# Performance work log

Hardware: AMD Instinct MI355X
Metric: run time of the kernel (lower is better)

Reference implementation:

```python
import jax, jax.numpy as jnp
import numpy as np

N = 50000      # nodes
E2 = 400000    # undirected edges
E = 2 * E2     # directed edges (each undirected edge in both directions)
DIN = 512      # input feature dim
DH = 128       # MLP hidden
C = 8          # num classes / BP channels


def setup_inputs() -> dict:
    key = jax.random.key(0)
    ks = jax.random.split(key, 9)
    x = jax.random.normal(ks[0], (N, DIN), jnp.float32)
    src0 = jax.random.randint(ks[1], (E2,), 0, N)
    dst0 = jax.random.randint(ks[2], (E2,), 0, N)
    # symmetric directed edge list: row 0 = source j, row 1 = target i
    edge_index = jnp.stack([jnp.concatenate([src0, dst0]),
                            jnp.concatenate([dst0, src0])])
    w0 = jax.random.uniform(ks[3], (E2,), jnp.float32, 0.5, 1.5)
    edge_weight = jnp.concatenate([w0, w0])  # reverse edge shares weight
    # edge_rv[e] = index of the reverse of edge e
    edge_rv = jnp.concatenate([jnp.arange(E2) + E2, jnp.arange(E2)])
    W1 = jax.random.normal(ks[4], (DIN, DH), jnp.float32) * 0.05
    b1 = jnp.zeros((DH,), jnp.float32)
    W2 = jax.random.normal(ks[5], (DH, C), jnp.float32) * 0.05
    b2 = jnp.zeros((C,), jnp.float32)
    param = jax.random.normal(ks[6], (C, C), jnp.float32) * 0.1
    return {"x": x, "edge_index": edge_index, "edge_weight": edge_weight,
            "edge_rv": edge_rv, "W1": W1, "b1": b1, "W2": W2, "b2": b2,
            "param": param, "K": 5}


def log_normalize(log_x):
    return log_x - jax.nn.logsumexp(log_x, axis=-1, keepdims=True)


def reference(x, edge_index, edge_weight, edge_rv, W1, b1, W2, b2, param, K):
    # MLP transform + LogSoftmax -> initial log-beliefs [N, C]
    h = jax.nn.relu(x @ W1 + b1)
    log_b0 = jax.nn.log_softmax(h @ W2 + b2, axis=-1)

    # learn_H=True: logH = logsigmoid(param + param^T), [C, C]
    logH = jax.nn.log_sigmoid(param + param.T)
    src, dst = edge_index[0], edge_index[1]
    # per-edge coupling matrix [E, C, C]
    logC = edge_weight[:, None, None] * logH[None, :, :]

    log_b = log_b0
    log_msg = None
    for _ in range(K):
        x_j = log_b[src]                       # gather source beliefs [E, C]
        if log_msg is not None:
            x_j = x_j - log_msg[edge_rv]       # remove reverse message
        # tropical-semiring matvec in log domain: logsumexp over source channel
        log_msg = log_normalize(jax.nn.logsumexp(x_j[:, :, None] + logC, axis=1))
        agg = jax.ops.segment_sum(log_msg, dst, num_segments=N)  # scatter-add
        log_b = log_normalize(log_b0 + agg)
    return log_b
```

## Files before the change

### kernel.cpp

```cpp
#include <hip/hip_runtime.h>
#include <hip/hip_bf16.h>
#include <math.h>

#define NN 50000
#define EE 800000
#define DINK 512
#define DHK 128
#define CK 8
#define KIT 5
#define NBLKS 196

typedef __attribute__((ext_vector_type(8))) short short8;
typedef __attribute__((ext_vector_type(4))) float f32x4;

__device__ __forceinline__ unsigned short f2bf(float f) {
    union { float f; unsigned int u; } v;
    v.f = f;
    unsigned int u = v.u;
    unsigned int r = (u + 0x7FFFu + ((u >> 16) & 1u)) >> 16;
    return (unsigned short)r;
}
__device__ __forceinline__ float bfu2f(unsigned int lo16) {
    union { unsigned int u; float f; } v;
    v.u = lo16 << 16;
    return v.f;
}

__global__ __launch_bounds__(64) void logH_kernel(const float* __restrict__ param,
                                                  float* __restrict__ logH) {
    int t = threadIdx.x;
    int i = t >> 3, j = t & 7;
    float z = param[i * 8 + j] + param[j * 8 + i];
    logH[t] = fminf(z, 0.0f) - log1pf(expf(-fabsf(z)));
}

__global__ __launch_bounds__(256) void w1t_kernel(const float* __restrict__ W1,
                                                  unsigned short* __restrict__ W1t) {
    int idx = blockIdx.x * 256 + threadIdx.x;
    int n = idx >> 9;
    int k = idx & 511;
    W1t[idx] = f2bf(W1[(size_t)k * DHK + n]);
}

__global__ __launch_bounds__(256) void mlp_mfma_kernel(
    const float* __restrict__ x, const unsigned short* __restrict__ W1t,
    const float* __restrict__ b1, const float* __restrict__ W2,
    const float* __restrict__ b2, float* __restrict__ logb0) {
    __shared__ unsigned short hs[128 * 136];
    __shared__ float W2s[128 * 8];
    __shared__ float b1s[128];
    __shared__ float b2s[8];

    const int tid = threadIdx.x;
    const int wave = tid >> 6;
    const int lane = tid & 63;
    const int q = lane >> 4;
    const int lm = lane & 15;
    const int wm = wave >> 1, wn = wave & 1;
    const int n0 = blockIdx.x * 128;

    if (tid < 128) b1s[tid] = b1[tid];
    if (tid < 8) b2s[tid] = b2[tid];
    {
        int i = tid * 4;
        *(float4*)&W2s[i] = *(const float4*)&W2[i];
    }
    __syncthreads();

    const float* xptr[4];
#pragma unroll
    for (int mt = 0; mt < 4; ++mt) {
        int r = n0 + wm * 64 + mt * 16 + lm;
        if (r > NN - 1) r = NN - 1;
        xptr[mt] = x + (size_t)r * DINK + q * 8;
    }
    const unsigned short* bptr[4];
#pragma unroll
    for (int nt = 0; nt < 4; ++nt) {
        int c = wn * 64 + nt * 16 + lm;
        bptr[nt] = W1t + (size_t)c * DINK + q * 8;
    }

    f32x4 acc[4][4];
#pragma unroll
    for (int mt = 0; mt < 4; ++mt)
#pragma unroll
        for (int nt = 0; nt < 4; ++nt) acc[mt][nt] = (f32x4){0.f, 0.f, 0.f, 0.f};

    float4 ar[4][2];
    short8 bc[4];
#pragma unroll
    for (int mt = 0; mt < 4; ++mt) {
        ar[mt][0] = *(const float4*)(xptr[mt]);
        ar[mt][1] = *(const float4*)(xptr[mt] + 4);
    }
#pragma unroll
    for (int nt = 0; nt < 4; ++nt) bc[nt] = *(const short8*)(bptr[nt]);

#pragma unroll
    for (int k0 = 32; k0 <= DINK; k0 += 32) {
        float4 ar2[4][2];
        short8 b2f[4];
        if (k0 < DINK) {
#pragma unroll
            for (int mt = 0; mt < 4; ++mt) {
                ar2[mt][0] = *(const float4*)(xptr[mt] + k0);
                ar2[mt][1] = *(const float4*)(xptr[mt] + k0 + 4);
            }
#pragma unroll
            for (int nt = 0; nt < 4; ++nt)
                b2f[nt] = *(const short8*)(bptr[nt] + k0);
        }
        short8 af[4];
#pragma unroll
        for (int mt = 0; mt < 4; ++mt) {
            union { short8 s; __hip_bfloat162 h[4]; } cv;
            cv.h[0] = __float22bfloat162_rn(make_float2(ar[mt][0].x, ar[mt][0].y));
            cv.h[1] = __float22bfloat162_rn(make_float2(ar[mt][0].z, ar[mt][0].w));
            cv.h[2] = __float22bfloat162_rn(make_float2(ar[mt][1].x, ar[mt][1].y));
            cv.h[3] = __float22bfloat162_rn(make_float2(ar[mt][1].z, ar[mt][1].w));
            af[mt] = cv.s;
        }
#pragma unroll
        for (int mt = 0; mt < 4; ++mt)
#pragma unroll
            for (int nt = 0; nt < 4; ++nt)
                acc[mt][nt] = __builtin_amdgcn_mfma_f32_16x16x32_bf16(
                    af[mt], bc[nt], acc[mt][nt], 0, 0, 0);
        if (k0 < DINK) {
#pragma unroll
            for (int mt = 0; mt < 4; ++mt) {
                ar[mt][0] = ar2[mt][0];
                ar[mt][1] = ar2[mt][1];
            }
#pragma unroll
            for (int nt = 0; nt < 4; ++nt) bc[nt] = b2f[nt];
        }
    }

#pragma unroll
    for (int nt = 0; nt < 4; ++nt) {
        int j = wn * 64 + nt * 16 + lm;
        float bj = b1s[j];
#pragma unroll
        for (int mt = 0; mt < 4; ++mt) {
            int rbase = wm * 64 + mt * 16 + q * 4;
#pragma unroll
            for (int r = 0; r < 4; ++r) {
                float h = fmaxf(acc[mt][nt][r] + bj, 0.0f);
                hs[(rbase + r) * 136 + j] = f2bf(h);
            }
        }
    }
    __syncthreads();

    int row = tid >> 1;
    int half = tid & 1;
    const unsigned short* hp = &hs[row * 136 + half * 64];
    float p[8] = {0.f, 0.f, 0.f, 0.f, 0.f, 0.f, 0.f, 0.f};
#pragma unroll
    for (int ch = 0; ch < 8; ++ch) {
        uint4 c4 = *(const uint4*)(hp + ch * 8);
        unsigned int uu[4] = {c4.x, c4.y, c4.z, c4.w};
#pragma unroll
        for (int p2 = 0; p2 < 4; ++p2) {
            float h0 = bfu2f(uu[p2] & 0xFFFFu);
            float h1 = bfu2f(uu[p2] >> 16);
            int j = half * 64 + ch * 8 + p2 * 2;
            const float* w0 = &W2s[j * 8];
            const float* w1 = &W2s[(j + 1) * 8];
#pragma unroll
            for (int c = 0; c < 8; ++c) p[c] = fmaf(h0, w0[c], p[c]);
#pragma unroll
            for (int c = 0; c < 8; ++c) p[c] = fmaf(h1, w1[c], p[c]);
        }
    }
#pragma unroll
    for (int c = 0; c < 8; ++c) p[c] += __shfl_xor(p[c], 1, 64);
    int grow = n0 + row;
    if (half == 0 && grow < NN) {
        float v[8];
        float mx = -1e30f;
#pragma unroll
        for (int c = 0; c < 8; ++c) {
            v[c] = p[c] + b2s[c];
            mx = fmaxf(mx, v[c]);
        }
        float s = 0.0f;
#pragma unroll
        for (int c = 0; c < 8; ++c) s += expf(v[c] - mx);
        float ln = mx + logf(s);
        float4* p0 = (float4*)&logb0[(size_t)grow * 8];
        p0[0] = make_float4(v[0] - ln, v[1] - ln, v[2] - ln, v[3] - ln);
        p0[1] = make_float4(v[4] - ln, v[5] - ln, v[6] - ln, v[7] - ln);
    }
}


__global__ __launch_bounds__(256) void deg_kernel(const int* __restrict__ dst,
                                                  int* __restrict__ cnt) {
    int e = blockIdx.x * 256 + threadIdx.x;
    if (e < EE) atomicAdd(&cnt[dst[e]], 1);
}

__global__ __launch_bounds__(256) void scan_partial_kernel(
    const int* __restrict__ cnt, int* __restrict__ partial) {
    __shared__ int sd[256];
    int t = threadIdx.x;
    int i = blockIdx.x * 256 + t;
    sd[t] = (i < NN) ? cnt[i] : 0;
    __syncthreads();
#pragma unroll
    for (int s = 128; s > 0; s >>= 1) {
        if (t < s) sd[t] += sd[t + s];
        __syncthreads();
    }
    if (t == 0) partial[blockIdx.x] = sd[0];
}

__global__ __launch_bounds__(256) void scan_tops_kernel(
    const int* __restrict__ partial, int* __restrict__ tops) {
    __shared__ int sd[256];
    int t = threadIdx.x;
    sd[t] = (t < NBLKS) ? partial[t] : 0;
    __syncthreads();
#pragma unroll
    for (int s = 1; s < 256; s <<= 1) {
        int a = sd[t];
        int b = (t >= s) ? sd[t - s] : 0;
        __syncthreads();
        sd[t] = a + b;
        __syncthreads();
    }
    if (t < NBLKS) tops[t] = (t > 0) ? sd[t - 1] : 0;
}

__global__ __launch_bounds__(256) void scan_write_kernel(
    const int* __restrict__ cnt, const int* __restrict__ tops,
    int* __restrict__ off) {
    __shared__ int sd[256];
    int t = threadIdx.x;
    int i = blockIdx.x * 256 + t;
    int v = (i < NN) ? cnt[i] : 0;
    sd[t] = v;
    __syncthreads();
#pragma unroll
    for (int s = 1; s < 256; s <<= 1) {
        int a = sd[t];
        int b = (t >= s) ? sd[t - s] : 0;
        __syncthreads();
        sd[t] = a + b;
        __syncthreads();
    }
    if (i < NN) off[i] = tops[blockIdx.x] + sd[t] - v;
    if (i == NN - 1) off[NN] = EE;
}

__global__ __launch_bounds__(256) void pos_kernel(
    const int* __restrict__ src, const int* __restrict__ dst,
    const float* __restrict__ ew, const int* __restrict__ off,
    int* __restrict__ cnt, int* __restrict__ pos,
    int2* __restrict__ perm_sw) {
    int e = blockIdx.x * 256 + threadIdx.x;
    if (e >= EE) return;
    int d = dst[e];
    int p = off[d] + atomicAdd(&cnt[d], 1);
    pos[e] = p;
    int2 sw;
    sw.x = src[e];
    sw.y = __float_as_int(ew[e]);
    perm_sw[p] = sw;
}

__global__ __launch_bounds__(256) void rvpos_kernel(const int* __restrict__ rv,
                                                    const int* __restrict__ pos,
                                                    int* __restrict__ perm_rvp) {
    int e = blockIdx.x * 256 + threadIdx.x;
    if (e >= EE) return;
    perm_rvp[pos[e]] = pos[rv[e]];
}

__global__ __launch_bounds__(256) void init_xin_kernel(
    const int2* __restrict__ perm_sw, const float* __restrict__ logb0,
    float* __restrict__ xin, float* __restrict__ perm_w) {
    int p = blockIdx.x * 256 + threadIdx.x;
    if (p >= EE) return;
    int2 sw = perm_sw[p];
    perm_w[p] = __int_as_float(sw.y);
    const float4* pb = (const float4*)&logb0[(size_t)sw.x * 8];
    float4 a = pb[0], b = pb[1];
    float4* po = (float4*)&xin[(size_t)p * 8];
    po[0] = a;
    po[1] = b;
}


__global__ __launch_bounds__(256) void edge_msg_kernel(
    const float* __restrict__ perm_w, const float* __restrict__ logH,
    const float* __restrict__ xin, float* __restrict__ msg_out) {
    __shared__ float lH[64];
    if (threadIdx.x < 64) lH[threadIdx.x] = logH[threadIdx.x];
    __syncthreads();
    int p = blockIdx.x * 256 + threadIdx.x;
    if (p >= EE) return;

    float w = perm_w[p];
    const float4* pb = (const float4*)&xin[(size_t)p * 8];
    float4 v0 = pb[0], v1 = pb[1];
    float xj[8] = {v0.x, v0.y, v0.z, v0.w, v1.x, v1.y, v1.z, v1.w};

    float M = xj[0];
#pragma unroll
    for (int c = 1; c < 8; ++c) M = fmaxf(M, xj[c]);
#pragma unroll
    for (int c = 0; c < 8; ++c) xj[c] -= M;

    float mg[8];
#pragma unroll
    for (int c2 = 0; c2 < 8; ++c2) {
        float ssum = 0.0f;
#pragma unroll
        for (int c1 = 0; c1 < 8; ++c1)
            ssum += __expf(fmaf(w, lH[c1 * 8 + c2], xj[c1]));
        mg[c2] = __logf(ssum);
    }
    float mm = mg[0];
#pragma unroll
    for (int c = 1; c < 8; ++c) mm = fmaxf(mm, mg[c]);
    float se = 0.0f;
#pragma unroll
    for (int c = 0; c < 8; ++c) se += __expf(mg[c] - mm);
    float ln = mm + __logf(se);

    float4* po = (float4*)&msg_out[(size_t)p * 8];
    po[0] = make_float4(mg[0] - ln, mg[1] - ln, mg[2] - ln, mg[3] - ln);
    po[1] = make_float4(mg[4] - ln, mg[5] - ln, mg[6] - ln, mg[7] - ln);
}

__global__ __launch_bounds__(256) void node_agg_kernel(
    const float* __restrict__ logb0, const int* __restrict__ off,
    const float* __restrict__ msg, const int* __restrict__ perm_rvp,
    float* __restrict__ xin, float* __restrict__ out, int write_out) {
    int t = blockIdx.x * 256 + threadIdx.x;
    int n = t >> 3;
    int c = t & 7;
    if (n >= NN) return;
    int j0 = off[n], j1 = off[n + 1];
    float a = logb0[(size_t)n * 8 + c];
    for (int j = j0; j < j1; ++j) a += msg[(size_t)j * 8 + c];
    float mx = a;
#pragma unroll
    for (int s = 1; s < 8; s <<= 1) mx = fmaxf(mx, __shfl_xor(mx, s, 8));
    float ex = __expf(a - mx);
    float sum = ex;
#pragma unroll
    for (int s = 1; s < 8; s <<= 1) sum += __shfl_xor(sum, s, 8);
    float v = a - (mx + __logf(sum));
    if (write_out) {
        out[(size_t)n * 8 + c] = v;
    } else {
        for (int j = j0; j < j1; ++j) {
            int r = perm_rvp[j];
            xin[(size_t)r * 8 + c] = v - msg[(size_t)j * 8 + c];
        }
    }
}

extern "C" void kernel_launch(void* const* d_in, const int* in_sizes, int n_in,
                              void* d_out, int out_size, void* d_ws, size_t ws_size,
                              hipStream_t stream) {
    const float* x = (const float*)d_in[0];
    const int* ei = (const int*)d_in[1];
    const float* ew = (const float*)d_in[2];
    const int* rv = (const int*)d_in[3];
    const float* W1 = (const float*)d_in[4];
    const float* b1 = (const float*)d_in[5];
    const float* W2 = (const float*)d_in[6];
    const float* b2 = (const float*)d_in[7];
    const float* param = (const float*)d_in[8];
    float* out = (float*)d_out;

    const int* src = ei;
    const int* dst = ei + EE;

    float* wsf = (float*)d_ws;
    float* logH = wsf;
    float* logb0 = logH + 64;
    float* msg = logb0 + (size_t)NN * 8;
    float* xin = msg + (size_t)EE * 8;
    float* perm_w = xin + (size_t)EE * 8;
    int* off = (int*)(perm_w + EE);
    int2* perm_sw = (int2*)(off + (NN + 1));
    int* perm_rvp = (int*)(perm_sw + EE);
    unsigned short* W1t = (unsigned short*)(perm_rvp + EE);
    int* pos = (int*)xin;
    int* cnt = pos + EE;
    int* partial = cnt + NN;
    int* tops = partial + NBLKS;

    logH_kernel<<<1, 64, 0, stream>>>(param, logH);
    w1t_kernel<<<256, 256, 0, stream>>>(W1, W1t);
    mlp_mfma_kernel<<<(NN + 127) / 128, 256, 0, stream>>>(x, W1t, b1, W2, b2,
                                                          logb0);

    const int EB = (EE + 255) / 256;

    hipMemsetAsync(cnt, 0, (size_t)NN * sizeof(int), stream);
    deg_kernel<<<EB, 256, 0, stream>>>(dst, cnt);
    scan_partial_kernel<<<NBLKS, 256, 0, stream>>>(cnt, partial);
    scan_tops_kernel<<<1, 256, 0, stream>>>(partial, tops);
    scan_write_kernel<<<NBLKS, 256, 0, stream>>>(cnt, tops, off);
    hipMemsetAsync(cnt, 0, (size_t)NN * sizeof(int), stream);
    pos_kernel<<<EB, 256, 0, stream>>>(src, dst, ew, off, cnt, pos, perm_sw);
    rvpos_kernel<<<EB, 256, 0, stream>>>(rv, pos, perm_rvp);
    init_xin_kernel<<<EB, 256, 0, stream>>>(perm_sw, logb0, xin, perm_w);

    for (int it = 0; it < KIT; ++it) {
        edge_msg_kernel<<<EB, 256, 0, stream>>>(perm_w, logH, xin, msg);
        node_agg_kernel<<<(NN * 8 + 255) / 256, 256, 0, stream>>>(
            logb0, off, msg, perm_rvp, xin, out, it == KIT - 1 ? 1 : 0);
    }
}
```

Baseline: 497.5 us.

## Fuse edge message computation into node aggregation with double-buffered edge inputs

Replaces the separate per-edge message kernel and per-node aggregation kernel with one node-centric kernel. Each of the 8 channel threads of a node recomputes that channel's message for every incoming edge, once for the aggregation and again when writing the reverse-edge inputs. The per-edge message normalization is dropped, because the per-edge constant cancels in the later normalizations. This removes the message buffer's global write and reads and one launch per iteration, and ping-pongs two edge-input buffers to avoid read/write races. In exchange, the exp/log work per edge is doubled, and each thread re-reads the 32-byte edge input.

After: 530.8 us. 1.07x slower.

```diff
diff --git a/kernel.cpp b/kernel.cpp
--- a/kernel.cpp
+++ b/kernel.cpp
@@ -294,60 +294,38 @@
     po[1] = b;
 }
 
-
-__global__ __launch_bounds__(256) void edge_msg_kernel(
-    const float* __restrict__ perm_w, const float* __restrict__ logH,
-    const float* __restrict__ xin, float* __restrict__ msg_out) {
-    __shared__ float lH[64];
-    if (threadIdx.x < 64) lH[threadIdx.x] = logH[threadIdx.x];
-    __syncthreads();
-    int p = blockIdx.x * 256 + threadIdx.x;
-    if (p >= EE) return;
-
-    float w = perm_w[p];
-    const float4* pb = (const float4*)&xin[(size_t)p * 8];
-    float4 v0 = pb[0], v1 = pb[1];
-    float xj[8] = {v0.x, v0.y, v0.z, v0.w, v1.x, v1.y, v1.z, v1.w};
-
-    float M = xj[0];
-#pragma unroll
-    for (int c = 1; c < 8; ++c) M = fmaxf(M, xj[c]);
-#pragma unroll
-    for (int c = 0; c < 8; ++c) xj[c] -= M;
-
-    float mg[8];
-#pragma unroll
-    for (int c2 = 0; c2 < 8; ++c2) {
-        float ssum = 0.0f;
-#pragma unroll
-        for (int c1 = 0; c1 < 8; ++c1)
-            ssum += __expf(fmaf(w, lH[c1 * 8 + c2], xj[c1]));
-        mg[c2] = __logf(ssum);
-    }
-    float mm = mg[0];
-#pragma unroll
-    for (int c = 1; c < 8; ++c) mm = fmaxf(mm, mg[c]);
-    float se = 0.0f;
-#pragma unroll
-    for (int c = 0; c < 8; ++c) se += __expf(mg[c] - mm);
-    float ln = mm + __logf(se);
-
-    float4* po = (float4*)&msg_out[(size_t)p * 8];
-    po[0] = make_float4(mg[0] - ln, mg[1] - ln, mg[2] - ln, mg[3] - ln);
-    po[1] = make_float4(mg[4] - ln, mg[5] - ln, mg[6] - ln, mg[7] - ln);
-}
-
-__global__ __launch_bounds__(256) void node_agg_kernel(
+__global__ __launch_bounds__(256) void bp_iter_kernel(
     const float* __restrict__ logb0, const int* __restrict__ off,
-    const float* __restrict__ msg, const int* __restrict__ perm_rvp,
-    float* __restrict__ xin, float* __restrict__ out, int write_out) {
+    const float* __restrict__ perm_w, const int* __restrict__ perm_rvp,
+    const float* __restrict__ logH, const float* __restrict__ xin,
+    float* __restrict__ xout, float* __restrict__ out, int write_out) {
     int t = blockIdx.x * 256 + threadIdx.x;
     int n = t >> 3;
     int c = t & 7;
     if (n >= NN) return;
+
+    float lHc[8];
+#pragma unroll
+    for (int c1 = 0; c1 < 8; ++c1) lHc[c1] = logH[c1 * 8 + c];
+
     int j0 = off[n], j1 = off[n + 1];
     float a = logb0[(size_t)n * 8 + c];
-    for (int j = j0; j < j1; ++j) a += msg[(size_t)j * 8 + c];
+
+    for (int j = j0; j < j1; ++j) {
+        float w = perm_w[j];
+        const float4* pb = (const float4*)&xin[(size_t)j * 8];
+        float4 v0 = pb[0], v1 = pb[1];
+        float xj[8] = {v0.x, v0.y, v0.z, v0.w, v1.x, v1.y, v1.z, v1.w};
+        float M = xj[0];
+#pragma unroll
+        for (int k = 1; k < 8; ++k) M = fmaxf(M, xj[k]);
+        float ssum = 0.0f;
+#pragma unroll
+        for (int c1 = 0; c1 < 8; ++c1)
+            ssum += __expf(fmaf(w, lHc[c1], xj[c1] - M));
+        a += M + __logf(ssum);
+    }
+
     float mx = a;
 #pragma unroll
     for (int s = 1; s < 8; s <<= 1) mx = fmaxf(mx, __shfl_xor(mx, s, 8));
@@ -356,13 +334,26 @@
 #pragma unroll
     for (int s = 1; s < 8; s <<= 1) sum += __shfl_xor(sum, s, 8);
     float v = a - (mx + __logf(sum));
+
     if (write_out) {
         out[(size_t)n * 8 + c] = v;
-    } else {
-        for (int j = j0; j < j1; ++j) {
-            int r = perm_rvp[j];
-            xin[(size_t)r * 8 + c] = v - msg[(size_t)j * 8 + c];
-        }
+        return;
+    }
+    for (int j = j0; j < j1; ++j) {
+        float w = perm_w[j];
+        const float4* pb = (const float4*)&xin[(size_t)j * 8];
+        float4 v0 = pb[0], v1 = pb[1];
+        float xj[8] = {v0.x, v0.y, v0.z, v0.w, v1.x, v1.y, v1.z, v1.w};
+        float M = xj[0];
+#pragma unroll
+        for (int k = 1; k < 8; ++k) M = fmaxf(M, xj[k]);
+        float ssum = 0.0f;
+#pragma unroll
+        for (int c1 = 0; c1 < 8; ++c1)
+            ssum += __expf(fmaf(w, lHc[c1], xj[c1] - M));
+        float mg = M + __logf(ssum);
+        int r = perm_rvp[j];
+        xout[(size_t)r * 8 + c] = v - mg;
     }
 }
 
@@ -386,14 +377,14 @@
     float* wsf = (float*)d_ws;
     float* logH = wsf;
     float* logb0 = logH + 64;
-    float* msg = logb0 + (size_t)NN * 8;
-    float* xin = msg + (size_t)EE * 8;
-    float* perm_w = xin + (size_t)EE * 8;
+    float* xinA = logb0 + (size_t)NN * 8;
+    float* xinB = xinA + (size_t)EE * 8;
+    float* perm_w = xinB + (size_t)EE * 8;
     int* off = (int*)(perm_w + EE);
     int2* perm_sw = (int2*)(off + (NN + 1));
     int* perm_rvp = (int*)(perm_sw + EE);
     unsigned short* W1t = (unsigned short*)(perm_rvp + EE);
-    int* pos = (int*)xin;
+    int* pos = (int*)xinA;
     int* cnt = pos + EE;
     int* partial = cnt + NN;
     int* tops = partial + NBLKS;
@@ -413,11 +404,15 @@
     hipMemsetAsync(cnt, 0, (size_t)NN * sizeof(int), stream);
     pos_kernel<<<EB, 256, 0, stream>>>(src, dst, ew, off, cnt, pos, perm_sw);
     rvpos_kernel<<<EB, 256, 0, stream>>>(rv, pos, perm_rvp);
-    init_xin_kernel<<<EB, 256, 0, stream>>>(perm_sw, logb0, xin, perm_w);
-
+    init_xin_kernel<<<EB, 256, 0, stream>>>(perm_sw, logb0, xinA, perm_w);
+
+    const int NB8 = (NN * 8 + 255) / 256;
+    float* cur = xinA;
+    float* nxt = xinB;
     for (int it = 0; it < KIT; ++it) {
-        edge_msg_kernel<<<EB, 256, 0, stream>>>(perm_w, logH, xin, msg);
-        node_agg_kernel<<<(NN * 8 + 255) / 256, 256, 0, stream>>>(
-            logb0, off, msg, perm_rvp, xin, out, it == KIT - 1 ? 1 : 0);
-    }
-}
+        bp_iter_kernel<<<NB8, 256, 0, stream>>>(
+            logb0, off, perm_w, perm_rvp, logH, cur, nxt, out,
+            it == KIT - 1 ? 1 : 0);
+        float* tmp = cur; cur = nxt; nxt = tmp;
+    }
+}
```

## Drop per-edge message normalization and split reverse-message scatter into an edge kernel

Applied to the files above, without the earlier changes.

The per-edge log-normalization of messages is removed; the max shift M is added back instead. Any per-edge constant offset cancels in the later per-node belief normalization and propagates consistently through the reverse-message subtraction, so the final output is unchanged. The per-node loop that wrote scattered 4-byte cavity values is replaced by an edge-parallel kernel. That kernel reads the node belief and the message with float4 loads and writes each reversed edge's input as two float4 stores, using a new perm_dst array filled in pos_kernel. This adds one kernel launch per iteration and extra belief/perm_dst buffers, and leaves messages unnormalized in scale.

Result: no change. 503.9 us (+1.3%).

```diff
diff --git a/kernel.cpp b/kernel.cpp
--- a/kernel.cpp
+++ b/kernel.cpp
@@ -260,7 +260,7 @@
     const int* __restrict__ src, const int* __restrict__ dst,
     const float* __restrict__ ew, const int* __restrict__ off,
     int* __restrict__ cnt, int* __restrict__ pos,
-    int2* __restrict__ perm_sw) {
+    int2* __restrict__ perm_sw, int* __restrict__ perm_dst) {
     int e = blockIdx.x * 256 + threadIdx.x;
     if (e >= EE) return;
     int d = dst[e];
@@ -270,6 +270,7 @@
     sw.x = src[e];
     sw.y = __float_as_int(ew[e]);
     perm_sw[p] = sw;
+    perm_dst[p] = d;
 }
 
 __global__ __launch_bounds__(256) void rvpos_kernel(const int* __restrict__ rv,
@@ -322,25 +323,18 @@
 #pragma unroll
         for (int c1 = 0; c1 < 8; ++c1)
             ssum += __expf(fmaf(w, lH[c1 * 8 + c2], xj[c1]));
-        mg[c2] = __logf(ssum);
-    }
-    float mm = mg[0];
-#pragma unroll
-    for (int c = 1; c < 8; ++c) mm = fmaxf(mm, mg[c]);
-    float se = 0.0f;
-#pragma unroll
-    for (int c = 0; c < 8; ++c) se += __expf(mg[c] - mm);
-    float ln = mm + __logf(se);
+        mg[c2] = M + __logf(ssum);
+    }
 
     float4* po = (float4*)&msg_out[(size_t)p * 8];
-    po[0] = make_float4(mg[0] - ln, mg[1] - ln, mg[2] - ln, mg[3] - ln);
-    po[1] = make_float4(mg[4] - ln, mg[5] - ln, mg[6] - ln, mg[7] - ln);
-}
-
-__global__ __launch_bounds__(256) void node_agg_kernel(
+    po[0] = make_float4(mg[0], mg[1], mg[2], mg[3]);
+    po[1] = make_float4(mg[4], mg[5], mg[6], mg[7]);
+}
+
+__global__ __launch_bounds__(256) void node_belief_kernel(
     const float* __restrict__ logb0, const int* __restrict__ off,
-    const float* __restrict__ msg, const int* __restrict__ perm_rvp,
-    float* __restrict__ xin, float* __restrict__ out, int write_out) {
+    const float* __restrict__ msg, float* __restrict__ belief,
+    float* __restrict__ out, int write_out) {
     int t = blockIdx.x * 256 + threadIdx.x;
     int n = t >> 3;
     int c = t & 7;
@@ -356,14 +350,25 @@
 #pragma unroll
     for (int s = 1; s < 8; s <<= 1) sum += __shfl_xor(sum, s, 8);
     float v = a - (mx + __logf(sum));
-    if (write_out) {
-        out[(size_t)n * 8 + c] = v;
-    } else {
-        for (int j = j0; j < j1; ++j) {
-            int r = perm_rvp[j];
-            xin[(size_t)r * 8 + c] = v - msg[(size_t)j * 8 + c];
-        }
-    }
+    if (write_out) out[(size_t)n * 8 + c] = v;
+    else belief[(size_t)n * 8 + c] = v;
+}
+
+__global__ __launch_bounds__(256) void edge_scatter_kernel(
+    const int* __restrict__ perm_dst, const int* __restrict__ perm_rvp,
+    const float* __restrict__ belief, const float* __restrict__ msg,
+    float* __restrict__ xin) {
+    int p = blockIdx.x * 256 + threadIdx.x;
+    if (p >= EE) return;
+    int d = perm_dst[p];
+    int r = perm_rvp[p];
+    const float4* pb = (const float4*)&belief[(size_t)d * 8];
+    float4 b0 = pb[0], b1 = pb[1];
+    const float4* pm = (const float4*)&msg[(size_t)p * 8];
+    float4 m0 = pm[0], m1 = pm[1];
+    float4* po = (float4*)&xin[(size_t)r * 8];
+    po[0] = make_float4(b0.x - m0.x, b0.y - m0.y, b0.z - m0.z, b0.w - m0.w);
+    po[1] = make_float4(b1.x - m1.x, b1.y - m1.y, b1.z - m1.z, b1.w - m1.w);
 }
 
 extern "C" void kernel_launch(void* const* d_in, const int* in_sizes, int n_in,
@@ -386,13 +391,15 @@
     float* wsf = (float*)d_ws;
     float* logH = wsf;
     float* logb0 = logH + 64;
-    float* msg = logb0 + (size_t)NN * 8;
+    float* belief = logb0 + (size_t)NN * 8;
+    float* msg = belief + (size_t)NN * 8;
     float* xin = msg + (size_t)EE * 8;
     float* perm_w = xin + (size_t)EE * 8;
     int* off = (int*)(perm_w + EE);
     int2* perm_sw = (int2*)(off + (NN + 1));
     int* perm_rvp = (int*)(perm_sw + EE);
-    unsigned short* W1t = (unsigned short*)(perm_rvp + EE);
+    int* perm_dst = perm_rvp + EE;
+    unsigned short* W1t = (unsigned short*)(perm_dst + EE);
     int* pos = (int*)xin;
     int* cnt = pos + EE;
     int* partial = cnt + NN;
@@ -411,13 +418,19 @@
     scan_tops_kernel<<<1, 256, 0, stream>>>(partial, tops);
     scan_write_kernel<<<NBLKS, 256, 0, stream>>>(cnt, tops, off);
     hipMemsetAsync(cnt, 0, (size_t)NN * sizeof(int), stream);
-    pos_kernel<<<EB, 256, 0, stream>>>(src, dst, ew, off, cnt, pos, perm_sw);
+    pos_kernel<<<EB, 256, 0, stream>>>(src, dst, ew, off, cnt, pos, perm_sw,
+                                       perm_dst);
     rvpos_kernel<<<EB, 256, 0, stream>>>(rv, pos, perm_rvp);
     init_xin_kernel<<<EB, 256, 0, stream>>>(perm_sw, logb0, xin, perm_w);
 
+    const int NB8 = (NN * 8 + 255) / 256;
     for (int it = 0; it < KIT; ++it) {
+        int last = (it == KIT - 1) ? 1 : 0;
         edge_msg_kernel<<<EB, 256, 0, stream>>>(perm_w, logH, xin, msg);
-        node_agg_kernel<<<(NN * 8 + 255) / 256, 256, 0, stream>>>(
-            logb0, off, msg, perm_rvp, xin, out, it == KIT - 1 ? 1 : 0);
-    }
-}
+        node_belief_kernel<<<NB8, 256, 0, stream>>>(logb0, off, msg, belief,
+                                                    out, last);
+        if (!last)
+            edge_scatter_kernel<<<EB, 256, 0, stream>>>(perm_dst, perm_rvp,
+                                                        belief, msg, xin);
+    }
+}
```
